# Kernel tuning notes

Measured on AMD Instinct MI355X. Metric: run time of the kernel, lower is better.

The kernel has to match this reference:

```python
import jax, jax.numpy as jnp
import numpy as np

EMBED_DIM = 1024
NUM_HEADS = 16
HEAD_DIM = EMBED_DIM // NUM_HEADS


def setup_inputs() -> dict:
    key = jax.random.key(0)
    k_x, k_wqkv, k_bqkv, k_wo, k_bo = jax.random.split(key, 5)
    B, T, C = 4, 2048, EMBED_DIM
    # PyTorch Linear default init scale ~ 1/sqrt(fan_in); use small normals
    s = 1.0 / np.sqrt(C)
    return {
        "x": jax.random.normal(k_x, (B, T, C), dtype=jnp.float32),
        "w_qkv": jax.random.normal(k_wqkv, (C, 3 * C), dtype=jnp.float32) * s,
        "b_qkv": jax.random.normal(k_bqkv, (3 * C,), dtype=jnp.float32) * s,
        "w_out": jax.random.normal(k_wo, (C, C), dtype=jnp.float32) * s,
        "b_out": jax.random.normal(k_bo, (C,), dtype=jnp.float32) * s,
    }


def reference(x, w_qkv, b_qkv, w_out, b_out):
    B, T, C = x.shape
    H, D = NUM_HEADS, HEAD_DIM
    qkv = x @ w_qkv + b_qkv                      # (B, T, 3C)
    q, k, v = jnp.split(qkv, 3, axis=-1)
    # (B, H, T, D)
    q = q.reshape(B, T, H, D).transpose(0, 2, 1, 3)
    k = k.reshape(B, T, H, D).transpose(0, 2, 1, 3)
    v = v.reshape(B, T, H, D).transpose(0, 2, 1, 3)
    scores = jnp.einsum("bhqd,bhkd->bhqk", q, k) / jnp.sqrt(jnp.float32(D))
    causal = jnp.tril(jnp.ones((T, T), dtype=bool))  # (T, T)
    scores = jnp.where(causal[None, None, :, :], scores, -jnp.inf)
    attn = jax.nn.softmax(scores, axis=-1)
    out = jnp.einsum("bhqk,bhkd->bhqd", attn, v)  # (B, H, T, D)
    out = out.transpose(0, 2, 1, 3).reshape(B, T, C)
    return out @ w_out + b_out
```

## Files before the change

kernel.cpp:

```cpp
#include <hip/hip_runtime.h>
#include <hip/hip_bf16.h>

#define B_  4
#define T_  2048
#define C_  1024
#define H_  16
#define D_  64
#define BH_ (B_*H_)

typedef float  f32x4  __attribute__((ext_vector_type(4)));
typedef __bf16 bf16x8 __attribute__((ext_vector_type(8)));
typedef __bf16 bf16x2 __attribute__((ext_vector_type(2)));

static __device__ __forceinline__ ushort f2bf(float f) {
    union { float f; unsigned u; } x; x.f = f;
    unsigned r = ((x.u >> 16) & 1u) + 0x7fffu;
    return (ushort)((x.u + r) >> 16);
}

static __device__ __forceinline__ uint packbf(float a, float b) {
    bf16x2 v = { (__bf16)a, (__bf16)b };
    return __builtin_bit_cast(uint, v);
}

static __device__ __forceinline__ void gload_lds16(const void* g, void* l) {
    __builtin_amdgcn_global_load_lds(
        (const __attribute__((address_space(1))) unsigned int*)g,
        (__attribute__((address_space(3))) unsigned int*)l, 16, 0, 0);
}

template<int N> static __device__ __forceinline__ void waitcnt_vm() {
    if constexpr (N == 0) asm volatile("s_waitcnt vmcnt(0)" ::: "memory");
    else if constexpr (N == 3) asm volatile("s_waitcnt vmcnt(3)" ::: "memory");
    else if constexpr (N == 4) asm volatile("s_waitcnt vmcnt(4)" ::: "memory");
    else static_assert(N == 0 || N == 3 || N == 4);
    __builtin_amdgcn_sched_barrier(0);
}
static __device__ __forceinline__ void lgkm0() {
    asm volatile("s_waitcnt lgkmcnt(0)" ::: "memory");
    __builtin_amdgcn_sched_barrier(0);
}

__global__ void cvt_kernel(const float* __restrict__ in, ushort* __restrict__ out, int n) {
    int i = (blockIdx.x * blockDim.x + threadIdx.x) * 4;
    if (i < n) {
        float4 v = *(const float4*)(in + i);
        ushort4 o;
        o.x = f2bf(v.x); o.y = f2bf(v.y); o.z = f2bf(v.z); o.w = f2bf(v.w);
        *(ushort4*)(out + i) = o;
    }
}

__global__ void transpose_cvt_kernel(const float* __restrict__ in, ushort* __restrict__ out,
                                     int K, int N) {
    __shared__ float tile[32][33];
    int k0 = blockIdx.y * 32, n0 = blockIdx.x * 32;
    int tx = threadIdx.x & 31, ty = threadIdx.x >> 5;
    #pragma unroll
    for (int r = 0; r < 32; r += 8)
        tile[ty + r][tx] = in[(size_t)(k0 + ty + r) * N + n0 + tx];
    __syncthreads();
    #pragma unroll
    for (int r = 0; r < 32; r += 8)
        out[(size_t)(n0 + ty + r) * K + k0 + tx] = f2bf(tile[tx][ty + r]);
}

template<int NFR, bool QKV>
__global__ __launch_bounds__(512, 2) void gemm_hk(
    const ushort* __restrict__ A,
    const ushort* __restrict__ Bt,
    const float*  __restrict__ bias,
    void* __restrict__ outp,
    ushort* __restrict__ vtp)
{
    constexpr int NT   = 16;
    constexpr int BN   = NFR * 64;
    constexpr int ABUF = 32768;
    constexpr int BBUF = BN * 128;
    constexpr int LB   = (NFR == 4) ? 2 : 1;
    constexpr int PK   = 2 + LB;
    __shared__ __align__(16) char lds[2 * ABUF + 2 * BBUF];
    char* ldsB = lds + 2 * ABUF;

    const int gX   = gridDim.x;
    const int orig = blockIdx.y * gX + blockIdx.x;
    const int cpx  = (gX * gridDim.y) >> 3;
    const int wg   = (orig & 7) * cpx + (orig >> 3);
    const int m0 = (wg / gX) * 256, n0 = (wg % gX) * BN;

    const int tid = threadIdx.x, lane = tid & 63;
    const int wv = tid >> 6, wm = wv >> 2, wn = wv & 3;
    const int lr = lane & 15, lh = lane >> 4;

    const int sc = (tid & 3) ^ ((tid >> 2) & 3);
    const ushort* aA = A  + (size_t)(m0 + (tid >> 2)) * 1024 + sc * 8;
    const ushort* aB = Bt + (size_t)(n0 + (tid >> 2)) * 1024 + sc * 8;

    const int cxor = (lh ^ (lr & 3)) * 16;
    const int arow = (wm * 128 + lr) * 64 + cxor;
    const int brow = (wn * (NFR * 16) + lr) * 64 + cxor;

    f32x4 acc[8][NFR] = {};

    auto stage_a = [&](int buf, int t, int kh) {
        #pragma unroll
        for (int p = 0; p < 2; ++p)
            gload_lds16(aA + (size_t)p * 131072 + t * 64 + kh * 32,
                        lds + buf * ABUF + kh * 16384 + p * 8192 + tid * 16);
    };
    auto stage_b = [&](int buf, int t, int kh) {
        #pragma unroll
        for (int p = 0; p < LB; ++p)
            gload_lds16(aB + (size_t)p * 131072 + t * 64 + kh * 32,
                        ldsB + buf * BBUF + kh * (BBUF / 2) + p * 8192 + tid * 16);
    };
    auto read_a = [&](bf16x8 (&af)[8], int buf, int kh) {
        const char* base = lds + buf * ABUF + kh * 16384 + arow;
        #pragma unroll
        for (int mi = 0; mi < 8; ++mi) af[mi] = *(const bf16x8*)(base + mi * 1024);
    };
    auto read_b = [&](bf16x8& b0, bf16x8& b1, int buf, int kh, int nh) {
        const char* base = ldsB + buf * BBUF + kh * (BBUF / 2) + brow + nh * 2048;
        b0 = *(const bf16x8*)(base);
        b1 = *(const bf16x8*)(base + 1024);
    };

#define MFMA2(NI, BB0, BB1)                                                          \
    do {                                                                             \
        __builtin_amdgcn_s_setprio(1);                                               \
        _Pragma("unroll")                                                            \
        for (int mi = 0; mi < 8; ++mi) {                                             \
            acc[mi][NI]     = __builtin_amdgcn_mfma_f32_16x16x32_bf16(af[mi], BB0,   \
                                                     acc[mi][NI], 0, 0, 0);          \
            acc[mi][NI + 1] = __builtin_amdgcn_mfma_f32_16x16x32_bf16(af[mi], BB1,   \
                                                     acc[mi][NI + 1], 0, 0, 0);      \
        }                                                                            \
        __builtin_amdgcn_s_setprio(0);                                               \
    } while (0)

    stage_a(0, 0, 0); stage_b(0, 0, 0);
    stage_a(0, 0, 1); stage_b(0, 0, 1);
    waitcnt_vm<PK>();
    __builtin_amdgcn_s_barrier();

    for (int t = 0; t < NT; ++t) {
        const int cur = t & 1, nxt = cur ^ 1;
        const bool pf = (t + 1 < NT);
        bf16x8 af[8], b0, b1;
        if constexpr (NFR == 4) {
            read_a(af, cur, 0); read_b(b0, b1, cur, 0, 0);
            if (pf) stage_a(nxt, t + 1, 0);
            __builtin_amdgcn_s_barrier();
            lgkm0();
            MFMA2(0, b0, b1);
            read_b(b0, b1, cur, 0, 1);
            if (pf) stage_b(nxt, t + 1, 0);
            if (t < NT - 1) waitcnt_vm<4>(); else waitcnt_vm<0>();
            __builtin_amdgcn_s_barrier();
            lgkm0();
            MFMA2(2, b0, b1);
            read_a(af, cur, 1); read_b(b0, b1, cur, 1, 0);
            if (pf) stage_a(nxt, t + 1, 1);
            __builtin_amdgcn_s_barrier();
            lgkm0();
            MFMA2(0, b0, b1);
            read_b(b0, b1, cur, 1, 1);
            if (pf) stage_b(nxt, t + 1, 1);
            if (t < NT - 1) waitcnt_vm<4>();
            __builtin_amdgcn_s_barrier();
            lgkm0();
            MFMA2(2, b0, b1);
        } else {
            read_a(af, cur, 0); read_b(b0, b1, cur, 0, 0);
            if (pf) { stage_a(nxt, t + 1, 0); stage_b(nxt, t + 1, 0); }
            if (t < NT - 1) waitcnt_vm<3>(); else waitcnt_vm<0>();
            __builtin_amdgcn_s_barrier();
            lgkm0();
            MFMA2(0, b0, b1);
            read_a(af, cur, 1); read_b(b0, b1, cur, 1, 0);
            if (pf) { stage_a(nxt, t + 1, 1); stage_b(nxt, t + 1, 1); }
            if (t < NT - 1) waitcnt_vm<3>();
            __builtin_amdgcn_s_barrier();
            lgkm0();
            MFMA2(0, b0, b1);
        }
    }
#undef MFMA2

    #pragma unroll
    for (int mi = 0; mi < 8; ++mi) {
        #pragma unroll
        for (int ni = 0; ni < NFR; ++ni) {
            int col = n0 + wn * (NFR * 16) + ni * 16 + lr;
            float bv = bias[col];
            if constexpr (QKV) {
                ushort* qkv = (ushort*)outp;
                int which = col >> 10;
                int h = (col & 1023) >> 6;
                int d = col & 63;
                if (which == 2) {
                    #pragma unroll
                    for (int r = 0; r < 4; ++r) {
                        int row = m0 + wm * 128 + mi * 16 + lh * 4 + r;
                        int b = row >> 11, tt = row & 2047;
                        vtp[(((size_t)(b * H_ + h)) * D_ + d) * T_ + tt] =
                            f2bf(acc[mi][ni][r] + bv);
                    }
                } else {
                    #pragma unroll
                    for (int r = 0; r < 4; ++r) {
                        int row = m0 + wm * 128 + mi * 16 + lh * 4 + r;
                        int b = row >> 11, tt = row & 2047;
                        float v = acc[mi][ni][r] + bv;
                        if (which == 0) v *= 0.18033688011112042f;
                        qkv[(size_t)which * (BH_ * T_ * D_) +
                            (((size_t)(b * H_ + h)) * T_ + tt) * D_ + d] = f2bf(v);
                    }
                }
            } else {
                float* Cout = (float*)outp;
                #pragma unroll
                for (int r = 0; r < 4; ++r) {
                    int row = m0 + wm * 128 + mi * 16 + lh * 4 + r;
                    Cout[(size_t)row * C_ + col] = acc[mi][ni][r] + bv;
                }
            }
        }
    }
}

__global__ __launch_bounds__(256, 4) void flash_kernel(
    const ushort* __restrict__ qb,
    const ushort* __restrict__ kb,
    const ushort* __restrict__ vt,
    ushort* __restrict__ ob)
{
    __shared__ __align__(16) ushort sK[2][64 * 64];
    __shared__ __align__(16) ushort sV[2][64 * 64];
    const int wg  = ((blockIdx.x & 7) << 7) | (blockIdx.x >> 3);
    const int bh  = wg >> 4;
    const int pr  = wg & 15;
    const int qtA = pr, qtB = 31 - pr;
    const int lane = threadIdx.x & 63, wv = threadIdx.x >> 6;
    const int lr = lane & 15, lh = lane >> 4;

    const ushort* qrowA = qb + ((size_t)bh * T_ + qtA * 64 + wv * 16 + lr) * D_;
    const ushort* qrowB = qb + ((size_t)bh * T_ + qtB * 64 + wv * 16 + lr) * D_;
    bf16x8 qfA0 = *(const bf16x8*)(qrowA + lh * 8);
    bf16x8 qfA1 = *(const bf16x8*)(qrowA + 32 + lh * 8);
    bf16x8 qfB0 = *(const bf16x8*)(qrowB + lh * 8);
    bf16x8 qfB1 = *(const bf16x8*)(qrowB + 32 + lh * 8);

    const int srow = lane >> 3;
    const int scol = ((lane & 7) ^ srow) * 8;
    const ushort* kbase = kb + (size_t)bh * T_ * D_;
    const ushort* vbase = vt + (size_t)bh * D_ * T_;

    const int swv  = (lr & 7) << 4;
    const int off0 = (16 * lh) ^ swv;
    const int off1 = (64 + 16 * lh) ^ swv;

    f32x4 oA[4] = {}, oB[4] = {};
    float mA = -1e30f, lA = 0.f, mB = -1e30f, lB = 0.f;

    auto redmax = [&](float x) {
        x = fmaxf(x, __int_as_float(__builtin_amdgcn_ds_swizzle(__float_as_int(x), 0x401F)));
        x = fmaxf(x, __shfl_xor(x, 32, 64));
        return x;
    };
    auto redsum = [&](float x) {
        x += __int_as_float(__builtin_amdgcn_ds_swizzle(__float_as_int(x), 0x401F));
        x += __shfl_xor(x, 32, 64);
        return x;
    };

    auto tile = [&](f32x4 (&o)[4], float& mrow, float& lsum,
                    const bf16x8& q0f, const bf16x8& q1f,
                    const char* K0, const char* V0, bool diag) {
        f32x4 s[4];
        __builtin_amdgcn_s_setprio(1);
        #pragma unroll
        for (int nt = 0; nt < 4; ++nt) {
            const int kk  = ((lr >> 2) << 3) | (lr & 3) | ((nt & 1) << 2) | ((nt >> 1) << 5);
            const int swk = (kk & 7) << 4;
            const char* krow = K0 + kk * 128;
            bf16x8 k0 = *(const bf16x8*)(krow + ((16 * lh) ^ swk));
            bf16x8 k1 = *(const bf16x8*)(krow + ((64 + 16 * lh) ^ swk));
            f32x4 a = {0.f, 0.f, 0.f, 0.f};
            a = __builtin_amdgcn_mfma_f32_16x16x32_bf16(k0, q0f, a, 0, 0, 0);
            a = __builtin_amdgcn_mfma_f32_16x16x32_bf16(k1, q1f, a, 0, 0, 0);
            s[nt] = a;
        }
        __builtin_amdgcn_s_setprio(0);
        if (diag) {
            #pragma unroll
            for (int nt = 0; nt < 4; ++nt) {
                const int kb0 = 8 * lh + 4 * (nt & 1) + 32 * (nt >> 1);
                #pragma unroll
                for (int r = 0; r < 4; ++r)
                    if (kb0 + r > wv * 16 + lr) s[nt][r] = -INFINITY;
            }
        }

        float pmax = fmaxf(fmaxf(fmaxf(s[0][0], s[0][1]), fmaxf(s[0][2], s[0][3])),
                           fmaxf(fmaxf(s[1][0], s[1][1]), fmaxf(s[1][2], s[1][3])));
        pmax = fmaxf(pmax, fmaxf(fmaxf(fmaxf(s[2][0], s[2][1]), fmaxf(s[2][2], s[2][3])),
                                 fmaxf(fmaxf(s[3][0], s[3][1]), fmaxf(s[3][2], s[3][3]))));
        pmax = redmax(pmax);

        if (__any(pmax > mrow + 8.f)) {
            float mnew = fmaxf(mrow, pmax);
            float al = __builtin_exp2f(mrow - mnew);
            lsum *= al;
            #pragma unroll
            for (int r = 0; r < 4; ++r) {
                float ar = __shfl(al, lh * 20 + r, 64);
                o[0][r] *= ar; o[1][r] *= ar; o[2][r] *= ar; o[3][r] *= ar;
            }
            mrow = mnew;
        }

        float rsum = 0.f;
        uint pk[8];
        #pragma unroll
        for (int nt = 0; nt < 4; ++nt) {
            float p0 = __builtin_exp2f(s[nt][0] - mrow);
            float p1 = __builtin_exp2f(s[nt][1] - mrow);
            float p2 = __builtin_exp2f(s[nt][2] - mrow);
            float p3 = __builtin_exp2f(s[nt][3] - mrow);
            rsum += (p0 + p1) + (p2 + p3);
            pk[nt * 2]     = packbf(p0, p1);
            pk[nt * 2 + 1] = packbf(p2, p3);
        }
        lsum += redsum(rsum);

        uint4 w0 = {pk[0], pk[1], pk[2], pk[3]};
        uint4 w1 = {pk[4], pk[5], pk[6], pk[7]};
        bf16x8 pf0 = __builtin_bit_cast(bf16x8, w0);
        bf16x8 pf1 = __builtin_bit_cast(bf16x8, w1);

        __builtin_amdgcn_s_setprio(1);
        #pragma unroll
        for (int dt = 0; dt < 4; ++dt) {
            const char* vrow = V0 + (dt * 16 + lr) * 128;
            bf16x8 v0 = *(const bf16x8*)(vrow + off0);
            bf16x8 v1 = *(const bf16x8*)(vrow + off1);
            o[dt] = __builtin_amdgcn_mfma_f32_16x16x32_bf16(pf0, v0, o[dt], 0, 0, 0);
            o[dt] = __builtin_amdgcn_mfma_f32_16x16x32_bf16(pf1, v1, o[dt], 0, 0, 0);
        }
        __builtin_amdgcn_s_setprio(0);
    };

    #pragma unroll
    for (int i = 0; i < 2; ++i) {
        int j = i * 4 + wv;
        gload_lds16(kbase + (size_t)(j * 8 + srow) * D_ + scol, &sK[0][j * 512]);
        gload_lds16(vbase + (size_t)(j * 8 + srow) * T_ + scol, &sV[0][j * 512]);
    }
    __syncthreads();

    for (int kt = 0; kt <= qtB; ++kt) {
        const int cur = kt & 1;
        if (kt < qtB) {
            const int nb = cur ^ 1;
            #pragma unroll
            for (int i = 0; i < 2; ++i) {
                int j = i * 4 + wv;
                gload_lds16(kbase + (size_t)((kt + 1) * 64 + j * 8 + srow) * D_ + scol, &sK[nb][j * 512]);
                gload_lds16(vbase + (size_t)(j * 8 + srow) * T_ + (kt + 1) * 64 + scol, &sV[nb][j * 512]);
            }
        }
        const char* K0 = (const char*)sK[cur];
        const char* V0 = (const char*)sV[cur];
        if (kt <= qtA) tile(oA, mA, lA, qfA0, qfA1, K0, V0, kt == qtA);
        tile(oB, mB, lB, qfB0, qfB1, K0, V0, kt == qtB);
        __syncthreads();
    }

    const int b = bh >> 4, h = bh & 15;
    auto writeout = [&](f32x4 (&o)[4], float lsum, int q0) {
        float inv = 1.f / lsum;
        #pragma unroll
        for (int r = 0; r < 4; ++r) {
            float ir = __shfl(inv, lh * 20 + r, 64);
            int q = q0 + lh * 4 + r;
            #pragma unroll
            for (int dt = 0; dt < 4; ++dt)
                ob[((size_t)b * T_ + q) * C_ + h * 64 + dt * 16 + lr] = f2bf(o[dt][r] * ir);
        }
    };
    writeout(oA, lA, qtA * 64 + wv * 16);
    writeout(oB, lB, qtB * 64 + wv * 16);
}

extern "C" void kernel_launch(void* const* d_in, const int* in_sizes, int n_in,
                              void* d_out, int out_size, void* d_ws, size_t ws_size,
                              hipStream_t stream) {
    const float* x     = (const float*)d_in[0];
    const float* w_qkv = (const float*)d_in[1];
    const float* b_qkv = (const float*)d_in[2];
    const float* w_out = (const float*)d_in[3];
    const float* b_out = (const float*)d_in[4];
    float* out = (float*)d_out;

    char* ws = (char*)d_ws;
    ushort* xb     = (ushort*)(ws + 0);
    ushort* wqkvT  = (ushort*)(ws + 16777216);
    ushort* woutT  = (ushort*)(ws + 23068672);
    ushort* qkv    = (ushort*)(ws + 25165824);
    ushort* vT     = (ushort*)(ws + 75497472);
    ushort* attn   = xb;
    ushort* qb = qkv;
    ushort* kb = qkv + (size_t)BH_ * T_ * D_;

    const int nx = B_ * T_ * C_;
    cvt_kernel<<<nx / 4 / 256, 256, 0, stream>>>(x, xb, nx);
    transpose_cvt_kernel<<<dim3(3 * C_ / 32, C_ / 32), 256, 0, stream>>>(w_qkv, wqkvT, C_, 3 * C_);
    transpose_cvt_kernel<<<dim3(C_ / 32, C_ / 32), 256, 0, stream>>>(w_out, woutT, C_, C_);
    gemm_hk<4, true><<<dim3(3 * C_ / 256, B_ * T_ / 256), 512, 0, stream>>>(xb, wqkvT, b_qkv, qkv, vT);
    flash_kernel<<<BH_ * 16, 256, 0, stream>>>(qb, kb, vT, attn);
    gemm_hk<2, false><<<dim3(C_ / 128, B_ * T_ / 256), 512, 0, stream>>>(attn, woutT, b_out, out, nullptr);
}
```

Before: 203.9 us.

## Replace QKV GEMM with simpler 128x128-tile kernel and raise flash occupancy

The QKV projection now runs in a new 128x128-tile, 256-thread GEMM with a single LDS buffer and plain syncthreads. It replaces the 256x256 double-buffered pipelined gemm_hk variant, and the QKV-specific paths are removed from gemm_hk. The new grid has 1536 workgroups instead of 384, which should balance better across CUs, but the kernel gives up global-load/MFMA overlap and reuses each tile less. The flash kernel's launch bound is also raised from 4 to 5 blocks per CU, which may increase register pressure or cause spills.

```diff
diff --git a/kernel.cpp b/kernel.cpp
--- a/kernel.cpp
+++ b/kernel.cpp
@@ -65,13 +65,90 @@
         out[(size_t)(n0 + ty + r) * K + k0 + tx] = f2bf(tile[tx][ty + r]);
 }
 
+__global__ __launch_bounds__(256) void gemm128_qkv(
+    const ushort* __restrict__ A,
+    const ushort* __restrict__ Bt,
+    const float*  __restrict__ bias,
+    ushort* __restrict__ qkv,
+    ushort* __restrict__ vtp)
+{
+    constexpr int K = 1024;
+    __shared__ __align__(16) ushort sA[128 * 64];
+    __shared__ __align__(16) ushort sB[128 * 64];
+    const int orig = blockIdx.y * 24 + blockIdx.x;
+    const int wg   = (orig & 7) * 192 + (orig >> 3);
+    const int m0 = (wg / 24) * 128, n0 = (wg % 24) * 128;
+    const int lane = threadIdx.x & 63, wv = threadIdx.x >> 6;
+    const int wm = wv >> 1, wn = wv & 1;
+    const int lr = lane & 15, lh = lane >> 4;
+    f32x4 acc[4][4] = {};
+
+    for (int kt = 0; kt < K; kt += 64) {
+        #pragma unroll
+        for (int i = 0; i < 4; ++i) {
+            int j = i * 4 + wv;
+            int p = j * 64 + lane;
+            int row = p >> 3, kc = (p & 7) << 3;
+            gload_lds16(A  + (size_t)(m0 + row) * K + kt + kc, &sA[j * 512]);
+            gload_lds16(Bt + (size_t)(n0 + row) * K + kt + kc, &sB[j * 512]);
+        }
+        __syncthreads();
+        #pragma unroll
+        for (int ks = 0; ks < 2; ++ks) {
+            bf16x8 af[4], bfr[4];
+            #pragma unroll
+            for (int mi = 0; mi < 4; ++mi)
+                af[mi] = *(const bf16x8*)&sA[(wm * 64 + mi * 16 + lr) * 64 + ks * 32 + lh * 8];
+            #pragma unroll
+            for (int ni = 0; ni < 4; ++ni)
+                bfr[ni] = *(const bf16x8*)&sB[(wn * 64 + ni * 16 + lr) * 64 + ks * 32 + lh * 8];
+            #pragma unroll
+            for (int mi = 0; mi < 4; ++mi)
+                #pragma unroll
+                for (int ni = 0; ni < 4; ++ni)
+                    acc[mi][ni] = __builtin_amdgcn_mfma_f32_16x16x32_bf16(af[mi], bfr[ni], acc[mi][ni], 0, 0, 0);
+        }
+        __syncthreads();
+    }
+
+    const int which = n0 >> 10;
+    #pragma unroll
+    for (int mi = 0; mi < 4; ++mi) {
+        #pragma unroll
+        for (int ni = 0; ni < 4; ++ni) {
+            int col = n0 + wn * 64 + ni * 16 + lr;
+            float bv = bias[col];
+            int h = (col & 1023) >> 6;
+            int d = col & 63;
+            if (which == 2) {
+                #pragma unroll
+                for (int r = 0; r < 4; ++r) {
+                    int row = m0 + wm * 64 + mi * 16 + lh * 4 + r;
+                    int b = row >> 11, tt = row & 2047;
+                    vtp[(((size_t)(b * H_ + h)) * D_ + d) * T_ + tt] =
+                        f2bf(acc[mi][ni][r] + bv);
+                }
+            } else {
+                #pragma unroll
+                for (int r = 0; r < 4; ++r) {
+                    int row = m0 + wm * 64 + mi * 16 + lh * 4 + r;
+                    int b = row >> 11, tt = row & 2047;
+                    float v = acc[mi][ni][r] + bv;
+                    if (which == 0) v *= 0.18033688011112042f;
+                    qkv[(size_t)which * (BH_ * T_ * D_) +
+                        (((size_t)(b * H_ + h)) * T_ + tt) * D_ + d] = f2bf(v);
+                }
+            }
+        }
+    }
+}
+
 template<int NFR, bool QKV>
 __global__ __launch_bounds__(512, 2) void gemm_hk(
     const ushort* __restrict__ A,
     const ushort* __restrict__ Bt,
     const float*  __restrict__ bias,
-    void* __restrict__ outp,
-    ushort* __restrict__ vtp)
+    void* __restrict__ outp)
 {
     constexpr int NT   = 16;
     constexpr int BN   = NFR * 64;
@@ -147,89 +224,38 @@
         const int cur = t & 1, nxt = cur ^ 1;
         const bool pf = (t + 1 < NT);
         bf16x8 af[8], b0, b1;
-        if constexpr (NFR == 4) {
-            read_a(af, cur, 0); read_b(b0, b1, cur, 0, 0);
-            if (pf) stage_a(nxt, t + 1, 0);
-            __builtin_amdgcn_s_barrier();
-            lgkm0();
-            MFMA2(0, b0, b1);
-            read_b(b0, b1, cur, 0, 1);
-            if (pf) stage_b(nxt, t + 1, 0);
-            if (t < NT - 1) waitcnt_vm<4>(); else waitcnt_vm<0>();
-            __builtin_amdgcn_s_barrier();
-            lgkm0();
-            MFMA2(2, b0, b1);
-            read_a(af, cur, 1); read_b(b0, b1, cur, 1, 0);
-            if (pf) stage_a(nxt, t + 1, 1);
-            __builtin_amdgcn_s_barrier();
-            lgkm0();
-            MFMA2(0, b0, b1);
-            read_b(b0, b1, cur, 1, 1);
-            if (pf) stage_b(nxt, t + 1, 1);
-            if (t < NT - 1) waitcnt_vm<4>();
-            __builtin_amdgcn_s_barrier();
-            lgkm0();
-            MFMA2(2, b0, b1);
-        } else {
-            read_a(af, cur, 0); read_b(b0, b1, cur, 0, 0);
-            if (pf) { stage_a(nxt, t + 1, 0); stage_b(nxt, t + 1, 0); }
-            if (t < NT - 1) waitcnt_vm<3>(); else waitcnt_vm<0>();
-            __builtin_amdgcn_s_barrier();
-            lgkm0();
-            MFMA2(0, b0, b1);
-            read_a(af, cur, 1); read_b(b0, b1, cur, 1, 0);
-            if (pf) { stage_a(nxt, t + 1, 1); stage_b(nxt, t + 1, 1); }
-            if (t < NT - 1) waitcnt_vm<3>();
-            __builtin_amdgcn_s_barrier();
-            lgkm0();
-            MFMA2(0, b0, b1);
-        }
+        read_a(af, cur, 0); read_b(b0, b1, cur, 0, 0);
+        if (pf) { stage_a(nxt, t + 1, 0); stage_b(nxt, t + 1, 0); }
+        if (t < NT - 1) waitcnt_vm<3>(); else waitcnt_vm<0>();
+        __builtin_amdgcn_s_barrier();
+        lgkm0();
+        MFMA2(0, b0, b1);
+        read_a(af, cur, 1); read_b(b0, b1, cur, 1, 0);
+        if (pf) { stage_a(nxt, t + 1, 1); stage_b(nxt, t + 1, 1); }
+        if (t < NT - 1) waitcnt_vm<3>();
+        __builtin_amdgcn_s_barrier();
+        lgkm0();
+        MFMA2(0, b0, b1);
     }
 #undef MFMA2
 
+    float* Cout = (float*)outp;
     #pragma unroll
     for (int mi = 0; mi < 8; ++mi) {
         #pragma unroll
         for (int ni = 0; ni < NFR; ++ni) {
             int col = n0 + wn * (NFR * 16) + ni * 16 + lr;
             float bv = bias[col];
-            if constexpr (QKV) {
-                ushort* qkv = (ushort*)outp;
-                int which = col >> 10;
-                int h = (col & 1023) >> 6;
-                int d = col & 63;
-                if (which == 2) {
-                    #pragma unroll
-                    for (int r = 0; r < 4; ++r) {
-                        int row = m0 + wm * 128 + mi * 16 + lh * 4 + r;
-                        int b = row >> 11, tt = row & 2047;
-                        vtp[(((size_t)(b * H_ + h)) * D_ + d) * T_ + tt] =
-                            f2bf(acc[mi][ni][r] + bv);
-                    }
-                } else {
-                    #pragma unroll
-                    for (int r = 0; r < 4; ++r) {
-                        int row = m0 + wm * 128 + mi * 16 + lh * 4 + r;
-                        int b = row >> 11, tt = row & 2047;
-                        float v = acc[mi][ni][r] + bv;
-                        if (which == 0) v *= 0.18033688011112042f;
-                        qkv[(size_t)which * (BH_ * T_ * D_) +
-                            (((size_t)(b * H_ + h)) * T_ + tt) * D_ + d] = f2bf(v);
-                    }
-                }
-            } else {
-                float* Cout = (float*)outp;
-                #pragma unroll
-                for (int r = 0; r < 4; ++r) {
-                    int row = m0 + wm * 128 + mi * 16 + lh * 4 + r;
-                    Cout[(size_t)row * C_ + col] = acc[mi][ni][r] + bv;
-                }
+            #pragma unroll
+            for (int r = 0; r < 4; ++r) {
+                int row = m0 + wm * 128 + mi * 16 + lh * 4 + r;
+                Cout[(size_t)row * C_ + col] = acc[mi][ni][r] + bv;
             }
         }
     }
 }
 
-__global__ __launch_bounds__(256, 4) void flash_kernel(
+__global__ __launch_bounds__(256, 5) void flash_kernel(
     const ushort* __restrict__ qb,
     const ushort* __restrict__ kb,
     const ushort* __restrict__ vt,
@@ -417,7 +443,7 @@
     cvt_kernel<<<nx / 4 / 256, 256, 0, stream>>>(x, xb, nx);
     transpose_cvt_kernel<<<dim3(3 * C_ / 32, C_ / 32), 256, 0, stream>>>(w_qkv, wqkvT, C_, 3 * C_);
     transpose_cvt_kernel<<<dim3(C_ / 32, C_ / 32), 256, 0, stream>>>(w_out, woutT, C_, C_);
-    gemm_hk<4, true><<<dim3(3 * C_ / 256, B_ * T_ / 256), 512, 0, stream>>>(xb, wqkvT, b_qkv, qkv, vT);
+    gemm128_qkv<<<dim3(24, 64), 256, 0, stream>>>(xb, wqkvT, b_qkv, qkv, vT);
     flash_kernel<<<BH_ * 16, 256, 0, stream>>>(qb, kb, vT, attn);
-    gemm_hk<2, false><<<dim3(C_ / 128, B_ * T_ / 256), 512, 0, stream>>>(attn, woutT, b_out, out, nullptr);
-}
+    gemm_hk<2, false><<<dim3(C_ / 128, B_ * T_ / 256), 512, 0, stream>>>(attn, woutT, b_out, out);
+}
```

Result: slower. 220.9 us (+8.3%).
